# Performance work log

Measured on AMD Instinct MI355X. Metric: run time of the kernel, lower is better.

Reference implementation:

```python
import jax, jax.numpy as jnp
from jax import lax
import numpy as np

NPOINT, RADIUS, NSAMPLE = 2048, 0.2, 32
EPS = 1e-5


def fps(xyz, npoint):
    # furthest point sampling; xyz [B,N,3] -> idx [B,npoint] int32
    B, N, _ = xyz.shape

    def body(carry, _):
        dist, far = carry  # dist [B,N], far [B]
        centroid = jnp.take_along_axis(xyz, far[:, None, None], axis=1)  # [B,1,3]
        d = jnp.sum((xyz - centroid) ** 2, -1)  # [B,N]
        dist = jnp.minimum(dist, d)
        nxt = jnp.argmax(dist, -1).astype(jnp.int32)
        return (dist, nxt), far

    init = (jnp.full((B, N), 1e10, xyz.dtype), jnp.zeros((B,), jnp.int32))
    _, idx = lax.scan(body, init, None, length=npoint)
    return jnp.transpose(idx)  # [B, npoint]


def ball_query(radius, nsample, xyz, new_xyz):
    # xyz [B,N,3], new_xyz [B,S,3] -> idx [B,S,nsample] int32
    B, N, _ = xyz.shape
    sqr = jnp.sum((new_xyz[:, :, None, :] - xyz[:, None, :, :]) ** 2, -1)  # [B,S,N]
    idx = jnp.broadcast_to(jnp.arange(N, dtype=jnp.int32), sqr.shape)
    idx = jnp.where(sqr > radius * radius, N, idx)
    idx = jnp.sort(idx, -1)[:, :, :nsample]  # first nsample in-ball indices
    first = idx[:, :, :1]
    return jnp.where(idx == N, first, idx)  # pad misses with first hit


def group(x, idx):
    # x [B,N,C], idx [B,S,K] -> [B,S,K,C]
    return jax.vmap(lambda xb, ib: xb[ib])(x, idx)


def setup_inputs() -> dict:
    key = jax.random.key(0)
    ks = jax.random.split(key, 8)
    B, N = 8, 8192
    mlp, in_c = [32, 32, 64], 6
    inp = {
        'xyz': jax.random.normal(ks[0], (B, N, 3), jnp.float32),
        'points': jax.random.normal(ks[1], (B, N, 3), jnp.float32),
    }
    cin = in_c
    for i, cout in enumerate(mlp):
        inp[f'w{i}'] = jax.random.normal(ks[2 + i], (cout, cin), jnp.float32) * (1.0 / np.sqrt(cin))
        inp[f'b{i}'] = jnp.zeros((cout,), jnp.float32)
        inp[f'g{i}'] = jnp.ones((cout,), jnp.float32)
        inp[f'be{i}'] = jnp.zeros((cout,), jnp.float32)
        cin = cout
    return inp


def reference(xyz, points, w0, b0, g0, be0, w1, b1, g1, be1, w2, b2, g2, be2):
    fps_idx = fps(xyz, NPOINT)
    new_xyz = jax.vmap(lambda xb, ib: xb[ib])(xyz, fps_idx)  # [B,S,3]
    idx = ball_query(RADIUS, NSAMPLE, xyz, new_xyz)  # [B,S,K]
    grouped_xyz = group(xyz, idx) - new_xyz[:, :, None, :]  # [B,S,K,3]
    feat = jnp.concatenate([grouped_xyz, group(points, idx)], -1)  # [B,S,K,6]
    for w, b, g, be in ((w0, b0, g0, be0), (w1, b1, g1, be1), (w2, b2, g2, be2)):
        feat = jnp.einsum('bskc,oc->bsko', feat, w) + b  # 1x1 conv
        mean = jnp.mean(feat, axis=(0, 1, 2))
        var = jnp.var(feat, axis=(0, 1, 2))
        feat = (feat - mean) * lax.rsqrt(var + EPS) * g + be  # BN (train stats)
        feat = jax.nn.relu(feat)
    new_points = jnp.max(feat, axis=2)  # max over neighborhood -> [B,S,64]
    return new_xyz, new_points
```

## Files before the change

kernel.cpp:

```cpp
#include <hip/hip_runtime.h>
#include <math.h>

#define BB 8
#define NN 8192
#define SS 2048
#define KK 32
#define NP (BB*SS*KK)
#define EPSF 1e-5f
#define TT 512

typedef float v2f __attribute__((ext_vector_type(2)));

template <int CTRL>
__device__ __forceinline__ double dpp_max_d(double key) {
    int lo = __double2loint(key), hi = __double2hiint(key);
    int nlo = __builtin_amdgcn_update_dpp(lo, lo, CTRL, 0xf, 0xf, false);
    int nhi = __builtin_amdgcn_update_dpp(hi, hi, CTRL, 0xf, 0xf, false);
    return fmax(__hiloint2double(nhi, nlo), key);
}

__device__ __forceinline__ double wave_max_key(double key) {
    key = dpp_max_d<0x111>(key);
    key = dpp_max_d<0x112>(key);
    key = dpp_max_d<0x114>(key);
    key = dpp_max_d<0x118>(key);
    key = dpp_max_d<0x142>(key);
    key = dpp_max_d<0x143>(key);
    return key;
}

__global__ __launch_bounds__(TT) void fps_kernel(const float* __restrict__ xyz,
                                                 float* __restrict__ out_newxyz) {
#pragma clang fp contract(off)
    const int PPT = NN / TT;
    const int NPAIR = PPT / 2;
    const int NW = TT / 64;
    int b = blockIdx.x;
    int t = threadIdx.x;
    int wid  = t >> 6;
    int lane = t & 63;
    const float* x = xyz + b * NN * 3;
    float* nout = out_newxyz + b * SS * 3;

    __shared__ float4 lxyz[NN];
    __shared__ __align__(16) double skey[2][NW];

    v2f px2[NPAIR], py2[NPAIR], pz2[NPAIR], d2[NPAIR];
    int lo_c[PPT];
#pragma unroll
    for (int s = 0; s < PPT; s++) lo_c[s] = (int)~(unsigned)(t + s * TT);
#pragma unroll
    for (int j = 0; j < NPAIR; j++) {
        int p0 = t + (2 * j) * TT;
        int p1 = p0 + TT;
        float ax = x[p0 * 3 + 0], ay = x[p0 * 3 + 1], az = x[p0 * 3 + 2];
        float bx = x[p1 * 3 + 0], by = x[p1 * 3 + 1], bz = x[p1 * 3 + 2];
        px2[j].x = ax; px2[j].y = bx;
        py2[j].x = ay; py2[j].y = by;
        pz2[j].x = az; pz2[j].y = bz;
        lxyz[p0] = make_float4(ax, ay, az, 0.f);
        lxyz[p1] = make_float4(bx, by, bz, 0.f);
        d2[j].x = 1e10f; d2[j].y = 1e10f;
    }
    __syncthreads();
    float4 c0 = lxyz[0];
    float cx = c0.x, cy = c0.y, cz = c0.z;

#pragma unroll 2
    for (int it = 0; it < SS; it++) {
        float sx = cx, sy = cy, sz = cz;
        if (t == 0) {
            nout[it * 3 + 0] = sx;
            nout[it * 3 + 1] = sy;
            nout[it * 3 + 2] = sz;
        }
        v2f cxx, cyy, czz;
        cxx.x = cx; cxx.y = cx;
        cyy.x = cy; cyy.y = cy;
        czz.x = cz; czz.y = cz;
        double acc[4] = {0.0, 0.0, 0.0, 0.0};
#pragma unroll
        for (int j = 0; j < NPAIR; j++) {
            v2f dx = px2[j] - cxx;
            v2f dy = py2[j] - cyy;
            v2f dz = pz2[j] - czz;
            v2f ss = (dx * dx + dy * dy) + dz * dz;
            v2f e  = __builtin_elementwise_min(d2[j], ss);
            d2[j] = e;
            double k0 = __hiloint2double(__float_as_int(e.x), lo_c[2 * j]);
            double k1 = __hiloint2double(__float_as_int(e.y), lo_c[2 * j + 1]);
            double kp = fmax(k0, k1);
            acc[j & 3] = fmax(acc[j & 3], kp);
        }
        double key = fmax(fmax(acc[0], acc[1]), fmax(acc[2], acc[3]));
        key = wave_max_key(key);
        if (lane == 63) skey[it & 1][wid] = key;
        __syncthreads();
        const double2* sk = (const double2*)&skey[it & 1][0];
        double2 k01 = sk[0];
        double2 k23 = sk[1];
        double2 k45 = sk[2];
        double2 k67 = sk[3];
        double ka = fmax(fmax(k01.x, k01.y), fmax(k23.x, k23.y));
        double kb = fmax(fmax(k45.x, k45.y), fmax(k67.x, k67.y));
        double k  = fmax(ka, kb);
        int gi = (int)(~(unsigned)__double2loint(k)) & (NN - 1);
        float4 c = lxyz[gi];
        cx = c.x; cy = c.y; cz = c.z;
    }
}

__global__ __launch_bounds__(256) void ballq_kernel(const float* __restrict__ xyz,
                                                    const float* __restrict__ new_xyz,
                                                    int* __restrict__ idx_out) {
    int q    = blockIdx.x * 4 + (threadIdx.x >> 6);
    int lane = threadIdx.x & 63;
    int b    = q >> 11;
    const float* x = xyz + b * NN * 3;
    const float* c = new_xyz + q * 3;
    float cx = c[0], cy = c[1], cz = c[2];
    int* out = idx_out + q * KK;
    const float R2 = (float)(0.2 * 0.2);

    int count = 0;
    int first = -1;
    unsigned long long below = (1ull << lane) - 1ull;
    for (int base = 0; base < NN; base += 128) {
        int p0 = base + 2 * lane;
        int p1 = p0 + 1;
        const float* xp = x + p0 * 3;
        float2 v01 = *(const float2*)(xp);
        float2 v23 = *(const float2*)(xp + 2);
        float2 v45 = *(const float2*)(xp + 4);
        float dx0 = __fsub_rn(v01.x, cx);
        float dy0 = __fsub_rn(v01.y, cy);
        float dz0 = __fsub_rn(v23.x, cz);
        float dx1 = __fsub_rn(v23.y, cx);
        float dy1 = __fsub_rn(v45.x, cy);
        float dz1 = __fsub_rn(v45.y, cz);
        float d0 = __fadd_rn(__fadd_rn(__fmul_rn(dx0, dx0), __fmul_rn(dy0, dy0)),
                             __fmul_rn(dz0, dz0));
        float d1 = __fadd_rn(__fadd_rn(__fmul_rn(dx1, dx1), __fmul_rn(dy1, dy1)),
                             __fmul_rn(dz1, dz1));
        bool in0 = !(d0 > R2);
        bool in1 = !(d1 > R2);
        unsigned long long m0 = __ballot(in0);
        unsigned long long m1 = __ballot(in1);
        if (first < 0 && (m0 | m1) != 0ull) {
            int c0 = m0 ? (2 * (__ffsll(m0) - 1))     : 9999;
            int c1 = m1 ? (2 * (__ffsll(m1) - 1) + 1) : 9999;
            first = base + (c0 < c1 ? c0 : c1);
        }
        int pre0 = __popcll(m0 & below) + __popcll(m1 & below);
        int pre1 = pre0 + (in0 ? 1 : 0);
        int pos0 = count + pre0;
        int pos1 = count + pre1;
        if (in0 && pos0 < KK) out[pos0] = p0;
        if (in1 && pos1 < KK) out[pos1] = p1;
        count += __popcll(m0) + __popcll(m1);
        if (count >= KK) break;
    }
    for (int i2 = count + lane; i2 < KK; i2 += 64) out[i2] = first;
}

__device__ __forceinline__ void load_in6(const float* __restrict__ xyz,
                                         const float* __restrict__ points,
                                         const float* __restrict__ new_xyz,
                                         const int* __restrict__ idx, int p, float inx[6]) {
    int bs = p >> 5;
    int b  = bs >> 11;
    int pt = idx[p];
    const float* xb = xyz + ((long)b * NN + pt) * 3;
    const float* pb = points + ((long)b * NN + pt) * 3;
    const float* nx = new_xyz + bs * 3;
    inx[0] = xb[0] - nx[0];
    inx[1] = xb[1] - nx[1];
    inx[2] = xb[2] - nx[2];
    inx[3] = pb[0];
    inx[4] = pb[1];
    inx[5] = pb[2];
}

template <int CIN, int COUT>
__device__ __forceinline__ void linear(const float* __restrict__ w,
                                       const float* __restrict__ bias,
                                       const float* xin, float* yout) {
#pragma unroll
    for (int o = 0; o < COUT; o++) {
        float acc = bias[o];
#pragma unroll
        for (int j = 0; j < CIN; j++) acc = fmaf(w[o * CIN + j], xin[j], acc);
        yout[o] = acc;
    }
}

template <int C>
__device__ __forceinline__ void bn_coef(const float* __restrict__ stats,
                                        const float* __restrict__ g,
                                        const float* __restrict__ be,
                                        float* s_sc, float* s_sh) {
    int t = threadIdx.x;
    if (t < C) {
        float mean = stats[t] * (1.0f / (float)NP);
        float var  = stats[C + t] * (1.0f / (float)NP) - mean * mean;
        float rstd = 1.0f / sqrtf(var + EPSF);
        float sc = g[t] * rstd;
        s_sc[t] = sc;
        s_sh[t] = be[t] - mean * sc;
    }
    __syncthreads();
}

template <int C>
__device__ __forceinline__ void accum_stats(const float* y, float* __restrict__ gstats) {
    __shared__ float buf[256][33];
    __shared__ float ps[2][8][33];
    int t = threadIdx.x;
    int ch  = t & 31;
    int seg = t >> 5;
#pragma unroll
    for (int h = 0; h < C / 32; h++) {
        __syncthreads();
#pragma unroll
        for (int c = 0; c < 32; c++) buf[t][c] = y[h * 32 + c];
        __syncthreads();
        float s = 0.f, sq = 0.f;
#pragma unroll
        for (int r = 0; r < 32; r++) {
            float v = buf[seg * 32 + r][ch];
            s += v;
            sq = fmaf(v, v, sq);
        }
        ps[0][seg][ch] = s;
        ps[1][seg][ch] = sq;
        __syncthreads();
        if (t < 32) {
            float S = 0.f, Q = 0.f;
#pragma unroll
            for (int g = 0; g < 8; g++) {
                S += ps[0][g][t];
                Q += ps[1][g][t];
            }
            atomicAdd(&gstats[h * 32 + t], S);
            atomicAdd(&gstats[C + h * 32 + t], Q);
        }
    }
}

__global__ __launch_bounds__(256) void l0_stats_kernel(
    const float* __restrict__ xyz, const float* __restrict__ points,
    const float* __restrict__ new_xyz, const int* __restrict__ idx,
    const float* __restrict__ w0, const float* __restrict__ b0_,
    float* __restrict__ stats0) {
    int p = blockIdx.x * 256 + threadIdx.x;
    float inx[6];
    load_in6(xyz, points, new_xyz, idx, p, inx);
    float y0[32];
    linear<6, 32>(w0, b0_, inx, y0);
    accum_stats<32>(y0, stats0);
}

__global__ __launch_bounds__(256) void l1_stats_kernel(
    const float* __restrict__ xyz, const float* __restrict__ points,
    const float* __restrict__ new_xyz, const int* __restrict__ idx,
    const float* __restrict__ w0, const float* __restrict__ b0_,
    const float* __restrict__ g0, const float* __restrict__ be0,
    const float* __restrict__ w1, const float* __restrict__ b1_,
    const float* __restrict__ stats0, float* __restrict__ stats1) {
    __shared__ float sc0[32], sh0[32];
    bn_coef<32>(stats0, g0, be0, sc0, sh0);
    int p = blockIdx.x * 256 + threadIdx.x;
    float inx[6];
    load_in6(xyz, points, new_xyz, idx, p, inx);
    float y0[32];
    linear<6, 32>(w0, b0_, inx, y0);
#pragma unroll
    for (int c = 0; c < 32; c++) y0[c] = fmaxf(fmaf(y0[c], sc0[c], sh0[c]), 0.f);
    float y1[32];
    linear<32, 32>(w1, b1_, y0, y1);
    accum_stats<32>(y1, stats1);
}

__global__ __launch_bounds__(256) void l2_stats_kernel(
    const float* __restrict__ xyz, const float* __restrict__ points,
    const float* __restrict__ new_xyz, const int* __restrict__ idx,
    const float* __restrict__ w0, const float* __restrict__ b0_,
    const float* __restrict__ g0, const float* __restrict__ be0,
    const float* __restrict__ w1, const float* __restrict__ b1_,
    const float* __restrict__ g1, const float* __restrict__ be1,
    const float* __restrict__ w2, const float* __restrict__ b2_,
    const float* __restrict__ stats0, const float* __restrict__ stats1,
    float* __restrict__ stats2) {
    __shared__ float sc0[32], sh0[32], sc1[32], sh1[32];
    bn_coef<32>(stats0, g0, be0, sc0, sh0);
    bn_coef<32>(stats1, g1, be1, sc1, sh1);
    int p = blockIdx.x * 256 + threadIdx.x;
    float inx[6];
    load_in6(xyz, points, new_xyz, idx, p, inx);
    float y0[32];
    linear<6, 32>(w0, b0_, inx, y0);
#pragma unroll
    for (int c = 0; c < 32; c++) y0[c] = fmaxf(fmaf(y0[c], sc0[c], sh0[c]), 0.f);
    float y1[32];
    linear<32, 32>(w1, b1_, y0, y1);
#pragma unroll
    for (int c = 0; c < 32; c++) y1[c] = fmaxf(fmaf(y1[c], sc1[c], sh1[c]), 0.f);
    float y2[64];
    linear<32, 64>(w2, b2_, y1, y2);
    accum_stats<64>(y2, stats2);
}

__global__ __launch_bounds__(256) void final_kernel(
    const float* __restrict__ xyz, const float* __restrict__ points,
    const float* __restrict__ new_xyz, const int* __restrict__ idx,
    const float* __restrict__ w0, const float* __restrict__ b0_,
    const float* __restrict__ g0, const float* __restrict__ be0,
    const float* __restrict__ w1, const float* __restrict__ b1_,
    const float* __restrict__ g1, const float* __restrict__ be1,
    const float* __restrict__ w2, const float* __restrict__ b2_,
    const float* __restrict__ g2, const float* __restrict__ be2,
    const float* __restrict__ stats0, const float* __restrict__ stats1,
    const float* __restrict__ stats2, float* __restrict__ out_points) {
    __shared__ float sc0[32], sh0[32], sc1[32], sh1[32], sc2[64], sh2[64];
    bn_coef<32>(stats0, g0, be0, sc0, sh0);
    bn_coef<32>(stats1, g1, be1, sc1, sh1);
    bn_coef<64>(stats2, g2, be2, sc2, sh2);
    int p = blockIdx.x * 256 + threadIdx.x;
    float inx[6];
    load_in6(xyz, points, new_xyz, idx, p, inx);
    float y0[32];
    linear<6, 32>(w0, b0_, inx, y0);
#pragma unroll
    for (int c = 0; c < 32; c++) y0[c] = fmaxf(fmaf(y0[c], sc0[c], sh0[c]), 0.f);
    float y1[32];
    linear<32, 32>(w1, b1_, y0, y1);
#pragma unroll
    for (int c = 0; c < 32; c++) y1[c] = fmaxf(fmaf(y1[c], sc1[c], sh1[c]), 0.f);
    float y2[64];
    linear<32, 64>(w2, b2_, y1, y2);
#pragma unroll
    for (int c = 0; c < 64; c++) {
        float v = fmaxf(fmaf(y2[c], sc2[c], sh2[c]), 0.f);
#pragma unroll
        for (int off = 1; off < 32; off <<= 1)
            v = fmaxf(v, __shfl_xor(v, off));
        y2[c] = v;
    }
    int lane = threadIdx.x & 63;
    if ((lane & 31) == 0) {
        int bs = p >> 5;
        float4* o = (float4*)(out_points + (long)bs * 64);
#pragma unroll
        for (int c4 = 0; c4 < 16; c4++)
            o[c4] = make_float4(y2[c4 * 4], y2[c4 * 4 + 1], y2[c4 * 4 + 2], y2[c4 * 4 + 3]);
    }
}

extern "C" void kernel_launch(void* const* d_in, const int* in_sizes, int n_in,
                              void* d_out, int out_size, void* d_ws, size_t ws_size,
                              hipStream_t stream) {
    (void)in_sizes; (void)n_in; (void)out_size; (void)ws_size;
    const float* xyz    = (const float*)d_in[0];
    const float* points = (const float*)d_in[1];
    const float* w0  = (const float*)d_in[2];
    const float* b0_ = (const float*)d_in[3];
    const float* g0  = (const float*)d_in[4];
    const float* be0 = (const float*)d_in[5];
    const float* w1  = (const float*)d_in[6];
    const float* b1_ = (const float*)d_in[7];
    const float* g1  = (const float*)d_in[8];
    const float* be1 = (const float*)d_in[9];
    const float* w2  = (const float*)d_in[10];
    const float* b2_ = (const float*)d_in[11];
    const float* g2  = (const float*)d_in[12];
    const float* be2 = (const float*)d_in[13];

    float* out        = (float*)d_out;
    float* out_newxyz = out;
    float* out_points = out + BB * SS * 3;

    int*   idx    = (int*)d_ws;
    float* stats  = (float*)d_ws + NP;
    float* stats0 = stats;
    float* stats1 = stats + 64;
    float* stats2 = stats + 128;

    hipMemsetAsync(stats, 0, 256 * sizeof(float), stream);

    fps_kernel<<<BB, TT, 0, stream>>>(xyz, out_newxyz);
    ballq_kernel<<<BB * SS / 4, 256, 0, stream>>>(xyz, out_newxyz, idx);
    l0_stats_kernel<<<NP / 256, 256, 0, stream>>>(xyz, points, out_newxyz, idx, w0, b0_, stats0);
    l1_stats_kernel<<<NP / 256, 256, 0, stream>>>(xyz, points, out_newxyz, idx,
                                                  w0, b0_, g0, be0, w1, b1_, stats0, stats1);
    l2_stats_kernel<<<NP / 256, 256, 0, stream>>>(xyz, points, out_newxyz, idx,
                                                  w0, b0_, g0, be0, w1, b1_, g1, be1,
                                                  w2, b2_, stats0, stats1, stats2);
    final_kernel<<<NP / 256, 256, 0, stream>>>(xyz, points, out_newxyz, idx,
                                               w0, b0_, g0, be0, w1, b1_, g1, be1,
                                               w2, b2_, g2, be2, stats0, stats1, stats2,
                                               out_points);
}
```

Measured before the change: 1.978 ms.

## Compute layer-0 BN stats from input moments, widen ball query, fold memset

Layer-0 batch-norm statistics are now derived algebraically from the first and second moments of the 6-channel input (27 sums) combined with w0 and b0. This replaces running the 32-channel linear layer and reducing 64 statistics. The ball query now loads four points per lane with float4 reads per 256-point step instead of two per 128. The stats memset moves into the FPS kernel to drop one launch. The moment-based variance may lose float precision compared with the direct computation.

Result: no change. 1.942 ms (-1.8%).

```diff
diff --git a/kernel.cpp b/kernel.cpp
--- a/kernel.cpp
+++ b/kernel.cpp
@@ -30,7 +30,8 @@
 }
 
 __global__ __launch_bounds__(TT) void fps_kernel(const float* __restrict__ xyz,
-                                                 float* __restrict__ out_newxyz) {
+                                                 float* __restrict__ out_newxyz,
+                                                 float* __restrict__ stats_zero) {
 #pragma clang fp contract(off)
     const int PPT = NN / TT;
     const int NPAIR = PPT / 2;
@@ -41,6 +42,8 @@
     int lane = t & 63;
     const float* x = xyz + b * NN * 3;
     float* nout = out_newxyz + b * SS * 3;
+
+    if (b == 0 && t < 256) stats_zero[t] = 0.f;
 
     __shared__ float4 lxyz[NN];
     __shared__ __align__(16) double skey[2][NW];
@@ -125,39 +128,48 @@
     int count = 0;
     int first = -1;
     unsigned long long below = (1ull << lane) - 1ull;
-    for (int base = 0; base < NN; base += 128) {
-        int p0 = base + 2 * lane;
-        int p1 = p0 + 1;
-        const float* xp = x + p0 * 3;
-        float2 v01 = *(const float2*)(xp);
-        float2 v23 = *(const float2*)(xp + 2);
-        float2 v45 = *(const float2*)(xp + 4);
-        float dx0 = __fsub_rn(v01.x, cx);
-        float dy0 = __fsub_rn(v01.y, cy);
-        float dz0 = __fsub_rn(v23.x, cz);
-        float dx1 = __fsub_rn(v23.y, cx);
-        float dy1 = __fsub_rn(v45.x, cy);
-        float dz1 = __fsub_rn(v45.y, cz);
-        float d0 = __fadd_rn(__fadd_rn(__fmul_rn(dx0, dx0), __fmul_rn(dy0, dy0)),
-                             __fmul_rn(dz0, dz0));
-        float d1 = __fadd_rn(__fadd_rn(__fmul_rn(dx1, dx1), __fmul_rn(dy1, dy1)),
-                             __fmul_rn(dz1, dz1));
-        bool in0 = !(d0 > R2);
-        bool in1 = !(d1 > R2);
+    for (int base = 0; base < NN; base += 256) {
+        int p0 = base + 4 * lane;
+        const float4* xp = (const float4*)(x + p0 * 3);
+        float4 A  = xp[0];
+        float4 Bv = xp[1];
+        float4 Cv = xp[2];
+        float dx0 = __fsub_rn(A.x,  cx), dy0 = __fsub_rn(A.y,  cy), dz0 = __fsub_rn(A.z,  cz);
+        float dx1 = __fsub_rn(A.w,  cx), dy1 = __fsub_rn(Bv.x, cy), dz1 = __fsub_rn(Bv.y, cz);
+        float dx2 = __fsub_rn(Bv.z, cx), dy2 = __fsub_rn(Bv.w, cy), dz2 = __fsub_rn(Cv.x, cz);
+        float dx3 = __fsub_rn(Cv.y, cx), dy3 = __fsub_rn(Cv.z, cy), dz3 = __fsub_rn(Cv.w, cz);
+        float d0 = __fadd_rn(__fadd_rn(__fmul_rn(dx0, dx0), __fmul_rn(dy0, dy0)), __fmul_rn(dz0, dz0));
+        float d1 = __fadd_rn(__fadd_rn(__fmul_rn(dx1, dx1), __fmul_rn(dy1, dy1)), __fmul_rn(dz1, dz1));
+        float d2 = __fadd_rn(__fadd_rn(__fmul_rn(dx2, dx2), __fmul_rn(dy2, dy2)), __fmul_rn(dz2, dz2));
+        float d3 = __fadd_rn(__fadd_rn(__fmul_rn(dx3, dx3), __fmul_rn(dy3, dy3)), __fmul_rn(dz3, dz3));
+        bool in0 = !(d0 > R2), in1 = !(d1 > R2), in2 = !(d2 > R2), in3 = !(d3 > R2);
         unsigned long long m0 = __ballot(in0);
         unsigned long long m1 = __ballot(in1);
-        if (first < 0 && (m0 | m1) != 0ull) {
-            int c0 = m0 ? (2 * (__ffsll(m0) - 1))     : 9999;
-            int c1 = m1 ? (2 * (__ffsll(m1) - 1) + 1) : 9999;
-            first = base + (c0 < c1 ? c0 : c1);
-        }
-        int pre0 = __popcll(m0 & below) + __popcll(m1 & below);
+        unsigned long long m2 = __ballot(in2);
+        unsigned long long m3 = __ballot(in3);
+        if (first < 0 && (m0 | m1 | m2 | m3) != 0ull) {
+            int c0 = m0 ? (4 * (__ffsll(m0) - 1))     : 99999;
+            int c1 = m1 ? (4 * (__ffsll(m1) - 1) + 1) : 99999;
+            int c2 = m2 ? (4 * (__ffsll(m2) - 1) + 2) : 99999;
+            int c3 = m3 ? (4 * (__ffsll(m3) - 1) + 3) : 99999;
+            int cma = c0 < c1 ? c0 : c1;
+            int cmb = c2 < c3 ? c2 : c3;
+            first = base + (cma < cmb ? cma : cmb);
+        }
+        int pre0 = __popcll(m0 & below) + __popcll(m1 & below)
+                 + __popcll(m2 & below) + __popcll(m3 & below);
         int pre1 = pre0 + (in0 ? 1 : 0);
+        int pre2 = pre1 + (in1 ? 1 : 0);
+        int pre3 = pre2 + (in2 ? 1 : 0);
         int pos0 = count + pre0;
         int pos1 = count + pre1;
+        int pos2 = count + pre2;
+        int pos3 = count + pre3;
         if (in0 && pos0 < KK) out[pos0] = p0;
-        if (in1 && pos1 < KK) out[pos1] = p1;
-        count += __popcll(m0) + __popcll(m1);
+        if (in1 && pos1 < KK) out[pos1] = p0 + 1;
+        if (in2 && pos2 < KK) out[pos2] = p0 + 2;
+        if (in3 && pos3 < KK) out[pos3] = p0 + 3;
+        count += __popcll(m0) + __popcll(m1) + __popcll(m2) + __popcll(m3);
         if (count >= KK) break;
     }
     for (int i2 = count + lane; i2 < KK; i2 += 64) out[i2] = first;
@@ -211,6 +223,45 @@
     __syncthreads();
 }
 
+__device__ __forceinline__ void bn_coef0_mom(const float* __restrict__ mom,
+                                             const float* __restrict__ w0,
+                                             const float* __restrict__ b0_,
+                                             const float* __restrict__ g,
+                                             const float* __restrict__ be,
+                                             float* s_sc, float* s_sh) {
+    int t = threadIdx.x;
+    if (t < 32) {
+        float w[6];
+#pragma unroll
+        for (int j = 0; j < 6; j++) w[j] = w0[t * 6 + j];
+        float sw = 0.f;
+#pragma unroll
+        for (int j = 0; j < 6; j++) sw = fmaf(w[j], mom[j], sw);
+        float bo = b0_[t];
+        float qf = 0.f;
+        int mi = 6;
+#pragma unroll
+        for (int j = 0; j < 6; j++) {
+#pragma unroll
+            for (int k = j; k < 6; k++) {
+                float ww = w[j] * w[k];
+                float f  = (j == k) ? 1.f : 2.f;
+                qf = fmaf(f * ww, mom[mi], qf);
+                mi++;
+            }
+        }
+        float sum   = sw + (float)NP * bo;
+        float sumsq = qf + 2.f * bo * sw + (float)NP * bo * bo;
+        float mean  = sum * (1.0f / (float)NP);
+        float var   = sumsq * (1.0f / (float)NP) - mean * mean;
+        float rstd  = 1.0f / sqrtf(var + EPSF);
+        float sc = g[t] * rstd;
+        s_sc[t] = sc;
+        s_sh[t] = be[t] - mean * sc;
+    }
+    __syncthreads();
+}
+
 template <int C>
 __device__ __forceinline__ void accum_stats(const float* y, float* __restrict__ gstats) {
     __shared__ float buf[256][33];
@@ -247,17 +298,39 @@
     }
 }
 
-__global__ __launch_bounds__(256) void l0_stats_kernel(
+__global__ __launch_bounds__(256) void l0_mom_kernel(
     const float* __restrict__ xyz, const float* __restrict__ points,
     const float* __restrict__ new_xyz, const int* __restrict__ idx,
-    const float* __restrict__ w0, const float* __restrict__ b0_,
-    float* __restrict__ stats0) {
-    int p = blockIdx.x * 256 + threadIdx.x;
+    float* __restrict__ mom) {
+    __shared__ float buf[256][33];
+    __shared__ float ps[8][33];
+    int t = threadIdx.x;
+    int p = blockIdx.x * 256 + t;
     float inx[6];
     load_in6(xyz, points, new_xyz, idx, p, inx);
-    float y0[32];
-    linear<6, 32>(w0, b0_, inx, y0);
-    accum_stats<32>(y0, stats0);
+#pragma unroll
+    for (int j = 0; j < 6; j++) buf[t][j] = inx[j];
+    int mi = 6;
+#pragma unroll
+    for (int j = 0; j < 6; j++) {
+#pragma unroll
+        for (int k = j; k < 6; k++) { buf[t][mi] = inx[j] * inx[k]; mi++; }
+    }
+#pragma unroll
+    for (int c = 27; c < 32; c++) buf[t][c] = 0.f;
+    __syncthreads();
+    int ch = t & 31, seg = t >> 5;
+    float s = 0.f;
+#pragma unroll
+    for (int r = 0; r < 32; r++) s += buf[seg * 32 + r][ch];
+    ps[seg][ch] = s;
+    __syncthreads();
+    if (t < 27) {
+        float S = 0.f;
+#pragma unroll
+        for (int g2 = 0; g2 < 8; g2++) S += ps[g2][t];
+        atomicAdd(&mom[t], S);
+    }
 }
 
 __global__ __launch_bounds__(256) void l1_stats_kernel(
@@ -266,9 +339,9 @@
     const float* __restrict__ w0, const float* __restrict__ b0_,
     const float* __restrict__ g0, const float* __restrict__ be0,
     const float* __restrict__ w1, const float* __restrict__ b1_,
-    const float* __restrict__ stats0, float* __restrict__ stats1) {
+    const float* __restrict__ mom, float* __restrict__ stats1) {
     __shared__ float sc0[32], sh0[32];
-    bn_coef<32>(stats0, g0, be0, sc0, sh0);
+    bn_coef0_mom(mom, w0, b0_, g0, be0, sc0, sh0);
     int p = blockIdx.x * 256 + threadIdx.x;
     float inx[6];
     load_in6(xyz, points, new_xyz, idx, p, inx);
@@ -289,10 +362,10 @@
     const float* __restrict__ w1, const float* __restrict__ b1_,
     const float* __restrict__ g1, const float* __restrict__ be1,
     const float* __restrict__ w2, const float* __restrict__ b2_,
-    const float* __restrict__ stats0, const float* __restrict__ stats1,
+    const float* __restrict__ mom, const float* __restrict__ stats1,
     float* __restrict__ stats2) {
     __shared__ float sc0[32], sh0[32], sc1[32], sh1[32];
-    bn_coef<32>(stats0, g0, be0, sc0, sh0);
+    bn_coef0_mom(mom, w0, b0_, g0, be0, sc0, sh0);
     bn_coef<32>(stats1, g1, be1, sc1, sh1);
     int p = blockIdx.x * 256 + threadIdx.x;
     float inx[6];
@@ -319,10 +392,10 @@
     const float* __restrict__ g1, const float* __restrict__ be1,
     const float* __restrict__ w2, const float* __restrict__ b2_,
     const float* __restrict__ g2, const float* __restrict__ be2,
-    const float* __restrict__ stats0, const float* __restrict__ stats1,
+    const float* __restrict__ mom, const float* __restrict__ stats1,
     const float* __restrict__ stats2, float* __restrict__ out_points) {
     __shared__ float sc0[32], sh0[32], sc1[32], sh1[32], sc2[64], sh2[64];
-    bn_coef<32>(stats0, g0, be0, sc0, sh0);
+    bn_coef0_mom(mom, w0, b0_, g0, be0, sc0, sh0);
     bn_coef<32>(stats1, g1, be1, sc1, sh1);
     bn_coef<64>(stats2, g2, be2, sc2, sh2);
     int p = blockIdx.x * 256 + threadIdx.x;
@@ -381,22 +454,20 @@
 
     int*   idx    = (int*)d_ws;
     float* stats  = (float*)d_ws + NP;
-    float* stats0 = stats;
+    float* mom    = stats;
     float* stats1 = stats + 64;
     float* stats2 = stats + 128;
 
-    hipMemsetAsync(stats, 0, 256 * sizeof(float), stream);
-
-    fps_kernel<<<BB, TT, 0, stream>>>(xyz, out_newxyz);
+    fps_kernel<<<BB, TT, 0, stream>>>(xyz, out_newxyz, stats);
     ballq_kernel<<<BB * SS / 4, 256, 0, stream>>>(xyz, out_newxyz, idx);
-    l0_stats_kernel<<<NP / 256, 256, 0, stream>>>(xyz, points, out_newxyz, idx, w0, b0_, stats0);
+    l0_mom_kernel<<<NP / 256, 256, 0, stream>>>(xyz, points, out_newxyz, idx, mom);
     l1_stats_kernel<<<NP / 256, 256, 0, stream>>>(xyz, points, out_newxyz, idx,
-                                                  w0, b0_, g0, be0, w1, b1_, stats0, stats1);
+                                                  w0, b0_, g0, be0, w1, b1_, mom, stats1);
     l2_stats_kernel<<<NP / 256, 256, 0, stream>>>(xyz, points, out_newxyz, idx,
                                                   w0, b0_, g0, be0, w1, b1_, g1, be1,
-                                                  w2, b2_, stats0, stats1, stats2);
+                                                  w2, b2_, mom, stats1, stats2);
     final_kernel<<<NP / 256, 256, 0, stream>>>(xyz, points, out_newxyz, idx,
                                                w0, b0_, g0, be0, w1, b1_, g1, be1,
-                                               w2, b2_, g2, be2, stats0, stats1, stats2,
+                                               w2, b2_, g2, be2, mom, stats1, stats2,
                                                out_points);
 }
```
